# Performance work log

Measured on AMD Instinct MI355X. Metric: run time of the kernel, lower is better.

Reference implementation:

```python
import jax, jax.numpy as jnp
import numpy as np
import math

B, N, D, H, K, W = 2, 2048, 512, 8, 64, 5
HD = D // H      # head_dim = 64
QC = HD // 4     # per-head quaternion component = 16
QI = D // 4      # full-model quaternion component = 128


def _qlinear(x, r, i, j, k, b):
    # Hamilton-product weight matrix, as built in QLinear.forward
    Wm = jnp.concatenate([
        jnp.concatenate([r, -i, -j, -k], 1),
        jnp.concatenate([i,  r, -k,  j], 1),
        jnp.concatenate([j,  k,  r, -i], 1),
        jnp.concatenate([k, -j,  i,  r], 1)], 0)
    return x @ Wm.T + b


def _layernorm(x, g, b, eps=1e-5):
    m = x.mean(-1, keepdims=True)
    v = ((x - m) ** 2).mean(-1, keepdims=True)
    return (x - m) / jnp.sqrt(v + eps) * g + b


def _forward(query, key, value, cross_context, density_feat, mask, time_idx,
             q_r, q_i, q_j, q_k, q_b, k_r, k_i, k_j, k_k, k_b,
             v_w, v_b, o_w, o_b, thr, dm1_w, dm1_b, dm2_w, dm2_b,
             ef, ec, ev_w, ev_b, ln_g, ln_b):
    spike_slope = 5.0
    # ---- QuaternionSpikeAttention (cross_ctx=True, dropout inactive in eval) ----
    q = _qlinear(query, q_r, q_i, q_j, q_k, q_b)
    k = _qlinear(key, k_r, k_i, k_j, k_k, k_b) + _qlinear(cross_context, k_r, k_i, k_j, k_k, k_b)
    v = jnp.concatenate([value, cross_context], -1) @ v_w.T + v_b
    qh = q.reshape(B, N, H, HD)
    kh = k.reshape(B, N, H, HD)
    vh = v.reshape(B, N, H, HD)
    # sum of the 4 quaternion-component dot products == full dot over head_dim
    scores = jnp.einsum('bmhd,bnhd->bhmn', qh, kh) / math.sqrt(QC)
    scores = jnp.clip(scores, -6.0, 6.0)
    base_thr = jax.nn.softplus(thr)
    hdm = jax.nn.gelu(density_feat @ dm1_w.T + dm1_b, approximate=False)
    d_shift = (hdm @ dm2_w.T + dm2_b)[..., 0]                # [B, N]
    threshold = base_thr + d_shift[:, None, None, :] * 0.1   # varies over key index
    gate = jax.nn.sigmoid(spike_slope * (scores - threshold))
    mod = scores * (1.0 + 2.0 * gate)
    m2 = mask[:, None, :, None] * mask[:, None, None, :]     # [B,1,M,N] outer mask
    mod = jnp.where(m2 == 0, -10000.0, mod)
    wts = jax.nn.softmax(jnp.clip(mod, -30.0, 30.0), axis=-1)
    attn = jnp.einsum('bhmn,bnhd->bmhd', wts, vh).reshape(B, N, D)
    attn = attn @ o_w.T + o_b
    # ---- TemporalEventConvolution ----
    order = jnp.argsort(time_idx, axis=1)
    qs = jnp.take_along_axis(query, order[..., None], axis=1)
    ms = jnp.take_along_axis(mask, order, axis=1)
    half = W // 2
    qp = jnp.pad(qs, ((0, 0), (half, half), (0, 0)))
    qwin = jnp.stack([qp[:, w:w + N] for w in range(W)], axis=2)  # [B,N,W,D]
    # quaternion-split filter matching collapses to a full dot over D
    act = jnp.einsum('bnwd,kwd->bnk', qwin, ef) / math.sqrt(QI)
    act = jnp.where(ms[..., None] == 0, -10000.0, act)
    act = jax.nn.softmax(act, axis=-1)
    ctx = act @ ec                                            # [B,N,D]
    ctx = _layernorm(ctx @ ev_w.T + ev_b, ln_g, ln_b) * ms[..., None]
    inv = jnp.argsort(order, axis=1)
    ctx = jnp.take_along_axis(ctx, inv[..., None], axis=1) * mask[..., None]
    return attn + ctx


def setup_inputs() -> dict:
    key0 = jax.random.key(0)
    ks = jax.random.split(key0, 24)
    lim = math.sqrt(6.0 / (QI + QI))
    def xav(k):
        return jax.random.uniform(k, (QI, QI), jnp.float32, -lim, lim)
    def lin(k, o, i):
        l = math.sqrt(1.0 / i)
        return jax.random.uniform(k, (o, i), jnp.float32, -l, l)
    return {
        'query': jax.random.normal(ks[0], (B, N, D), jnp.float32),
        'key': jax.random.normal(ks[1], (B, N, D), jnp.float32),
        'value': jax.random.normal(ks[2], (B, N, D), jnp.float32),
        'cross_context': jax.random.normal(ks[3], (B, N, D), jnp.float32),
        'density_feat': jax.random.normal(ks[4], (B, N, 3), jnp.float32),
        'mask': jnp.ones((B, N), jnp.float32),
        'time_idx': jax.random.randint(ks[5], (B, N), 0, 1000000),
        'q_r': xav(ks[6]), 'q_i': xav(ks[7]), 'q_j': xav(ks[8]), 'q_k': xav(ks[9]),
        'q_b': jnp.zeros((D,), jnp.float32),
        'k_r': xav(ks[10]), 'k_i': xav(ks[11]), 'k_j': xav(ks[12]), 'k_k': xav(ks[13]),
        'k_b': jnp.zeros((D,), jnp.float32),
        'v_w': lin(ks[14], D, 2 * D), 'v_b': jnp.zeros((D,), jnp.float32),
        'o_w': lin(ks[15], D, D), 'o_b': jnp.zeros((D,), jnp.float32),
        'thr': jnp.float32(-1.0),
        'dm1_w': lin(ks[16], 16, 3), 'dm1_b': jnp.zeros((16,), jnp.float32),
        'dm2_w': jnp.zeros((1, 16), jnp.float32), 'dm2_b': jnp.zeros((1,), jnp.float32),
        'ef': jax.random.normal(ks[17], (K, W, D), jnp.float32) * 0.02,
        'ec': jax.random.normal(ks[18], (K, D), jnp.float32) * 0.02,
        'ev_w': lin(ks[19], D, D), 'ev_b': jnp.zeros((D,), jnp.float32),
        'ln_g': jnp.ones((D,), jnp.float32), 'ln_b': jnp.zeros((D,), jnp.float32),
    }


def reference(query, key, value, cross_context, density_feat, mask, time_idx,
              q_r, q_i, q_j, q_k, q_b, k_r, k_i, k_j, k_k, k_b,
              v_w, v_b, o_w, o_b, thr, dm1_w, dm1_b, dm2_w, dm2_b,
              ef, ec, ev_w, ev_b, ln_g, ln_b):
    return _forward(query, key, value, cross_context, density_feat, mask, time_idx,
                    q_r, q_i, q_j, q_k, q_b, k_r, k_i, k_j, k_k, k_b,
                    v_w, v_b, o_w, o_b, thr, dm1_w, dm1_b, dm2_w, dm2_b,
                    ef, ec, ev_w, ev_b, ln_g, ln_b)
```

## Files before the change

kernel.cpp:

```cpp
#include <hip/hip_runtime.h>
#include <math.h>

#define BB 2
#define NN 2048
#define DDIM 512
#define HH 8
#define HDIM 64
#define BN 4096

#define WS_WMQ   0
#define WS_WMK   262144
#define WS_THRK  524288
#define WS_ORDER 528384
#define WS_DKW   532480
#define WS_W5    1843200
#define WS_Q     2105344
#define WS_K     4202496
#define WS_V     6299648
#define PLANE_US 2097152

typedef short bf16x8 __attribute__((ext_vector_type(8)));
typedef float f32x4  __attribute__((ext_vector_type(4)));

__device__ __forceinline__ float4 ld4(const float* p) { return *(const float4*)p; }

__device__ __forceinline__ float red16_sum(float v) {
  v += __shfl_xor(v, 1, 64);
  v += __shfl_xor(v, 2, 64);
  v += __shfl_xor(v, 4, 64);
  v += __shfl_xor(v, 8, 64);
  return v;
}

__device__ __forceinline__ unsigned short f2bu(float f) {
  unsigned u = __float_as_uint(f);
  unsigned r = 0x7FFFu + ((u >> 16) & 1u);
  return (unsigned short)((u + r) >> 16);
}
__device__ __forceinline__ float bu2f(unsigned short u) {
  return __uint_as_float(((unsigned)u) << 16);
}
__device__ __forceinline__ void split2(float x, unsigned short& hi, unsigned short& lo) {
  hi = f2bu(x);
  lo = f2bu(x - bu2f(hi));
}

__device__ __forceinline__ void build_wm_body(int idx,
    const float* qr, const float* qi, const float* qj, const float* qk,
    const float* kr, const float* ki, const float* kj, const float* kk,
    unsigned short* wmqH, unsigned short* wmqL,
    unsigned short* wmkH, unsigned short* wmkL)
{
  int sel = idx >> 18;
  int r   = idx & 262143;
  int p = r >> 9, q = r & 511;
  int pb = p >> 7, qb = q >> 7, pr = p & 127, qc = q & 127;
  const int   comp_t[4][4] = {{0,1,2,3},{1,0,3,2},{2,3,0,1},{3,2,1,0}};
  const float sign_t[4][4] = {{1.f,-1.f,-1.f,-1.f},{1.f,1.f,-1.f,1.f},
                              {1.f,1.f,1.f,-1.f},{1.f,-1.f,1.f,1.f}};
  const float* cq[4] = {qr,qi,qj,qk};
  const float* ck[4] = {kr,ki,kj,kk};
  int c = comp_t[pb][qb];
  float s = sign_t[pb][qb];
  const float* src = sel ? ck[c] : cq[c];
  float v = s * src[pr*128 + qc];
  unsigned short hi, lo;
  split2(v, hi, lo);
  if (sel) { wmkH[r] = hi; wmkL[r] = lo; }
  else     { wmqH[r] = hi; wmqL[r] = lo; }
}

__device__ __forceinline__ void presplit_body(int i, const float* src, int n4,
    unsigned short* hp, unsigned short* lp)
{
  if (i >= n4) return;
  float4 v = ((const float4*)src)[i];
  ushort4 h, l;
  split2(v.x, h.x, l.x);  split2(v.y, h.y, l.y);
  split2(v.z, h.z, l.z);  split2(v.w, h.w, l.w);
  ((ushort4*)hp)[i] = h;
  ((ushort4*)lp)[i] = l;
}

__device__ __forceinline__ void thr_body(int i,
    const float* df, const float* dm1w, const float* dm1b,
    const float* dm2w, const float* dm2b, const float* thrp,
    int dm1b_bstride, float* thrK)
{
  if (i >= BN) return;
  int b = i >> 11;
  const float* bb = dm1b + b*dm1b_bstride;
  float x0 = df[i*3+0], x1 = df[i*3+1], x2 = df[i*3+2];
  float acc = dm2b[0];
  #pragma unroll
  for (int j = 0; j < 16; j++) {
    float h = dm1w[j*3+0]*x0 + dm1w[j*3+1]*x1 + dm1w[j*3+2]*x2 + bb[j];
    h = 0.5f * h * (1.f + erff(h * 0.70710678118654752f));
    acc += h * dm2w[j];
  }
  float tv = thrp[0];
  float base = fmaxf(tv, 0.f) + log1pf(expf(-fabsf(tv)));
  thrK[i] = base + 0.1f * acc;
}

__global__ __launch_bounds__(256) void prologue_kernel(
    const float* __restrict__ qr, const float* __restrict__ qi,
    const float* __restrict__ qj, const float* __restrict__ qk,
    const float* __restrict__ kr, const float* __restrict__ ki,
    const float* __restrict__ kj, const float* __restrict__ kk,
    unsigned short* __restrict__ wmqH, unsigned short* __restrict__ wmqL,
    unsigned short* __restrict__ wmkH, unsigned short* __restrict__ wmkL,
    const float* __restrict__ query,
    unsigned short* __restrict__ qryH, unsigned short* __restrict__ qryL,
    const float* __restrict__ v_w,
    unsigned short* __restrict__ vwH, unsigned short* __restrict__ vwL,
    const float* __restrict__ o_w,
    unsigned short* __restrict__ owH, unsigned short* __restrict__ owL,
    const int* __restrict__ tidx, int* __restrict__ order,
    const float* __restrict__ df, const float* __restrict__ dm1w,
    const float* __restrict__ dm1b, const float* __restrict__ dm2w,
    const float* __restrict__ dm2b, const float* __restrict__ thrp,
    int dm1b_bstride, float* __restrict__ thrK,
    const float* __restrict__ ef, int efn4,
    unsigned short* __restrict__ efH, unsigned short* __restrict__ efL)
{
  __shared__ int ts[NN];
  int bx = blockIdx.x, t = threadIdx.x;
  if (bx < 2048) {
    build_wm_body(bx*256 + t, qr,qi,qj,qk, kr,ki,kj,kk, wmqH,wmqL, wmkH,wmkL);
  } else if (bx < 4096) {
    presplit_body((bx-2048)*256 + t, query, 524288, qryH, qryL);
  } else if (bx < 4608) {
    presplit_body((bx-4096)*256 + t, v_w, 131072, vwH, vwL);
  } else if (bx < 4864) {
    presplit_body((bx-4608)*256 + t, o_w, 65536, owH, owL);
  } else if (bx < 4880) {
    int r = bx - 4864;
    int b = r >> 3, blk = r & 7;
    for (int i = t; i < NN; i += 256) ts[i] = tidx[b*NN + i];
    __syncthreads();
    int i = blk*256 + t;
    int ti = ts[i];
    int rank = 0;
    #pragma unroll 4
    for (int j = 0; j < NN; j++) {
      int tj = ts[j];
      rank += (tj < ti || (tj == ti && j < i)) ? 1 : 0;
    }
    order[b*NN + rank] = i;
  } else if (bx < 4896) {
    thr_body((bx-4880)*256 + t, df, dm1w, dm1b, dm2w, dm2b, thrp,
             dm1b_bstride, thrK);
  } else {
    presplit_body((bx-4896)*256 + t, ef, efn4, efH, efL);
  }
}

__global__ __launch_bounds__(256) void presplit_kernel(
    const float* __restrict__ src, int n4,
    unsigned short* __restrict__ hp, unsigned short* __restrict__ lp)
{
  presplit_body(blockIdx.x*256 + threadIdx.x, src, n4, hp, lp);
}

#define GSTR 72
template<int MODE, int OUT, int AP, int BP>
__device__ __forceinline__ void mgemm_body(
    unsigned short* AHi, unsigned short* ALo,
    unsigned short* BHi, unsigned short* BLo,
    const float* __restrict__ A0, const float* __restrict__ A1,
    const unsigned short* __restrict__ APh, const unsigned short* __restrict__ APl,
    const float* __restrict__ W,
    const unsigned short* __restrict__ BPh, const unsigned short* __restrict__ BPl,
    const float* __restrict__ bias,
    float bias_scale, float scale, float* __restrict__ out,
    int Ka, int N, int ldout, int bx, int by)
{
  const int t = threadIdx.x;
  const int w = t >> 6, lane = t & 63;
  const int quad = lane >> 4, lm = lane & 15;
  const int m0 = bx * 64, n0 = by * 64;
  const int lrr = t >> 4, ld = (t & 15) * 4;

  f32x4 acc[4];
  #pragma unroll
  for (int s = 0; s < 4; s++) acc[s] = (f32x4){0.f,0.f,0.f,0.f};

  for (int k0 = 0; k0 < Ka; k0 += 64) {
    __syncthreads();
    if (AP) {
      #pragma unroll
      for (int i = 0; i < 2; i++) {
        int c = t*2 + i;
        int row = c >> 3, c8 = (c & 7) * 8;
        int off = (m0 + row)*Ka + k0 + c8;
        *(uint4*)&AHi[row*GSTR + c8] = *(const uint4*)&APh[off];
        *(uint4*)&ALo[row*GSTR + c8] = *(const uint4*)&APl[off];
      }
    } else {
      #pragma unroll
      for (int p = 0; p < 4; p++) {
        int row = lrr + p*16;
        float4 av;
        if (MODE == 0) {
          av = ld4(&A0[(size_t)(m0+row)*Ka + k0 + ld]);
        } else if (MODE == 1) {
          float4 x = ld4(&A0[(m0+row)*512 + k0 + ld]);
          float4 y = ld4(&A1[(m0+row)*512 + k0 + ld]);
          av = make_float4(x.x+y.x, x.y+y.y, x.z+y.z, x.w+y.w);
        } else {
          int kg = k0 + ld;
          av = (kg < 512) ? ld4(&A0[(m0+row)*512 + kg])
                          : ld4(&A1[(m0+row)*512 + kg - 512]);
        }
        ushort4 hi, lo;
        split2(av.x, hi.x, lo.x);  split2(av.y, hi.y, lo.y);
        split2(av.z, hi.z, lo.z);  split2(av.w, hi.w, lo.w);
        *(ushort4*)&AHi[row*GSTR + ld] = hi;
        *(ushort4*)&ALo[row*GSTR + ld] = lo;
      }
    }
    if (BP) {
      #pragma unroll
      for (int i = 0; i < 2; i++) {
        int c = t*2 + i;
        int row = c >> 3, c8 = (c & 7) * 8;
        int brow = n0 + row;  if (brow > N-1) brow = N-1;
        int off = brow*Ka + k0 + c8;
        *(uint4*)&BHi[row*GSTR + c8] = *(const uint4*)&BPh[off];
        *(uint4*)&BLo[row*GSTR + c8] = *(const uint4*)&BPl[off];
      }
    } else {
      #pragma unroll
      for (int p = 0; p < 4; p++) {
        int row = lrr + p*16;
        int brow = n0 + row;  if (brow > N-1) brow = N-1;
        float4 wv = ld4(&W[(size_t)brow*Ka + k0 + ld]);
        ushort4 hi, lo;
        split2(wv.x, hi.x, lo.x);  split2(wv.y, hi.y, lo.y);
        split2(wv.z, hi.z, lo.z);  split2(wv.w, hi.w, lo.w);
        *(ushort4*)&BHi[row*GSTR + ld] = hi;
        *(ushort4*)&BLo[row*GSTR + ld] = lo;
      }
    }
    __syncthreads();
    #pragma unroll
    for (int ks = 0; ks < 2; ks++) {
      int arow = (w*16 + lm)*GSTR + ks*32 + quad*8;
      bf16x8 ah = *(const bf16x8*)&AHi[arow];
      bf16x8 al = *(const bf16x8*)&ALo[arow];
      #pragma unroll
      for (int sub = 0; sub < 4; sub++) {
        int baddr = (sub*16 + lm)*GSTR + ks*32 + quad*8;
        bf16x8 bh = *(const bf16x8*)&BHi[baddr];
        bf16x8 bl = *(const bf16x8*)&BLo[baddr];
        acc[sub] = __builtin_amdgcn_mfma_f32_16x16x32_bf16(ah, bh, acc[sub], 0, 0, 0);
        acc[sub] = __builtin_amdgcn_mfma_f32_16x16x32_bf16(ah, bl, acc[sub], 0, 0, 0);
        acc[sub] = __builtin_amdgcn_mfma_f32_16x16x32_bf16(al, bh, acc[sub], 0, 0, 0);
      }
    }
  }
  #pragma unroll
  for (int sub = 0; sub < 4; sub++) {
    int col = n0 + sub*16 + lm;
    if (col >= N) continue;
    float bv = bias ? bias[col] * bias_scale : 0.f;
    if (OUT == 0) {
      #pragma unroll
      for (int r = 0; r < 4; r++) {
        int row = m0 + w*16 + quad*4 + r;
        out[(size_t)row*ldout + col] = acc[sub][r]*scale + bv;
      }
    } else if (OUT == 1) {
      unsigned short* hp = (unsigned short*)out;
      unsigned short* lp = hp + (size_t)4096*ldout;
      #pragma unroll
      for (int r = 0; r < 4; r++) {
        int row = m0 + w*16 + quad*4 + r;
        unsigned short hv, lv;
        split2(acc[sub][r]*scale + bv, hv, lv);
        hp[(size_t)row*ldout + col] = hv;
        lp[(size_t)row*ldout + col] = lv;
      }
    } else {
      unsigned short* hp = (unsigned short*)out;
      unsigned short* lp = hp + (size_t)PLANE_US;
      int hcol = col >> 6, d = col & 63;
      int row0 = m0 + w*16 + quad*4;
      int bb2 = row0 >> 11, n = row0 & 2047;
      unsigned short h0,h1,h2,h3,l0,l1,l2,l3;
      split2(acc[sub][0]*scale + bv, h0, l0);
      split2(acc[sub][1]*scale + bv, h1, l1);
      split2(acc[sub][2]*scale + bv, h2, l2);
      split2(acc[sub][3]*scale + bv, h3, l3);
      size_t vidx = (((size_t)bb2*8 + hcol)*64 + d)*2048 + n;
      *(ushort4*)&hp[vidx] = make_ushort4(h0,h1,h2,h3);
      *(ushort4*)&lp[vidx] = make_ushort4(l0,l1,l2,l3);
    }
  }
}

template<int MODE, int OUT, int AP, int BP>
__global__ __launch_bounds__(256) void mgemm_kernel(
    const float* __restrict__ A0, const float* __restrict__ A1,
    const unsigned short* __restrict__ APh, const unsigned short* __restrict__ APl,
    const float* __restrict__ W,
    const unsigned short* __restrict__ BPh, const unsigned short* __restrict__ BPl,
    const float* __restrict__ bias,
    float bias_scale, float scale, float* __restrict__ out,
    int Ka, int N, int ldout)
{
  __shared__ __align__(16) unsigned short AHi[64*GSTR], ALo[64*GSTR];
  __shared__ __align__(16) unsigned short BHi[64*GSTR], BLo[64*GSTR];
  mgemm_body<MODE,OUT,AP,BP>(AHi, ALo, BHi, BLo, A0, A1, APh, APl, W, BPh, BPl,
                             bias, bias_scale, scale, out, Ka, N, ldout,
                             blockIdx.x, blockIdx.y);
}

__global__ __launch_bounds__(256) void qkv_kernel(
    const unsigned short* __restrict__ qryH, const unsigned short* __restrict__ qryL,
    const unsigned short* __restrict__ wmqH, const unsigned short* __restrict__ wmqL,
    const float* __restrict__ q_b, float* __restrict__ Qb,
    const float* __restrict__ key_, const float* __restrict__ cross,
    const unsigned short* __restrict__ wmkH, const unsigned short* __restrict__ wmkL,
    const float* __restrict__ k_b, float* __restrict__ Kb,
    const float* __restrict__ value,
    const unsigned short* __restrict__ vwH, const unsigned short* __restrict__ vwL,
    const float* __restrict__ v_b, float* __restrict__ Vb,
    const unsigned short* __restrict__ efH, const unsigned short* __restrict__ efL,
    float rs128, int KW, float* __restrict__ dkwO)
{
  __shared__ __align__(16) unsigned short AHi[64*GSTR], ALo[64*GSTR];
  __shared__ __align__(16) unsigned short BHi[64*GSTR], BLo[64*GSTR];
  int by = blockIdx.y;
  if (by < 8) {
    mgemm_body<0,1,1,1>(AHi, ALo, BHi, BLo, nullptr, nullptr, qryH, qryL,
                        nullptr, wmqH, wmqL, q_b, 1.f, 1.f, Qb, 512, 512, 512,
                        blockIdx.x, by);
  } else if (by < 16) {
    mgemm_body<1,1,0,1>(AHi, ALo, BHi, BLo, key_, cross, nullptr, nullptr,
                        nullptr, wmkH, wmkL, k_b, 2.f, 1.f, Kb, 512, 512, 512,
                        blockIdx.x, by - 8);
  } else if (by < 24) {
    mgemm_body<2,2,0,1>(AHi, ALo, BHi, BLo, value, cross, nullptr, nullptr,
                        nullptr, vwH, vwL, v_b, 1.f, 1.f, Vb, 1024, 512, 512,
                        blockIdx.x, by - 16);
  } else {
    mgemm_body<0,0,1,1>(AHi, ALo, BHi, BLo, nullptr, nullptr, qryH, qryL,
                        nullptr, efH, efL, nullptr, 0.f, rs128, dkwO, 512, KW, KW,
                        blockIdx.x, by - 24);
  }
}

__global__ __launch_bounds__(256) void otail_kernel(
    const unsigned short* __restrict__ aH, const unsigned short* __restrict__ aL,
    const unsigned short* __restrict__ owH, const unsigned short* __restrict__ owL,
    const float* __restrict__ o_b, float* __restrict__ OutF,
    const float* __restrict__ dkw, const int* __restrict__ order,
    int K, int W, float* __restrict__ w5,
    const float* __restrict__ ec, const float* __restrict__ evw,
    float* __restrict__ ecv)
{
  __shared__ __align__(16) unsigned short AHi[64*GSTR], ALo[64*GSTR];
  __shared__ __align__(16) unsigned short BHi[64*GSTR], BLo[64*GSTR];
  int by = blockIdx.y;
  if (by < 8) {
    mgemm_body<0,0,1,1>(AHi, ALo, BHi, BLo, nullptr, nullptr, aH, aL,
                        nullptr, owH, owL, o_b, 1.f, 1.f, OutF, 512, 512, 512,
                        blockIdx.x, by);
  } else if (by == 8) {
    int KW = K*W, half = W >> 1;
    int total = BN*K;
    for (int idx = blockIdx.x*256 + threadIdx.x; idx < total; idx += 64*256) {
      int k  = idx % K;
      int bn = idx / K;
      int b = bn >> 11, r = bn & 2047;
      const int* ob = order + b*NN;
      float acc = 0.f;
      for (int w = 0; w < W; w++) {
        int rr = r + w - half;
        if (rr < 0 || rr >= NN) continue;
        acc += dkw[(size_t)(b*NN + ob[rr])*KW + k*W + w];
      }
      w5[(size_t)(b*NN + ob[r])*K + k] = acc;
    }
  } else {
    int total = K*512;
    for (int idx = blockIdx.x*256 + threadIdx.x; idx < total; idx += 64*256) {
      int k = idx >> 9, j = idx & 511;
      const float4* e4 = (const float4*)(ec + k*512);
      const float4* w4 = (const float4*)(evw + j*512);
      float acc = 0.f;
      for (int d = 0; d < 128; d++) {
        float4 a = e4[d], bv = w4[d];
        acc += a.x*bv.x + a.y*bv.y + a.z*bv.z + a.w*bv.w;
      }
      ecv[k*512 + j] = acc;
    }
  }
}

__global__ __launch_bounds__(256) void t2f_kernel(const float* __restrict__ w5raw,
    const float* __restrict__ ecv, const float* __restrict__ evb,
    const float* __restrict__ mask, int K, float* __restrict__ ctx2)
{
  int idx = blockIdx.x * 256 + threadIdx.x;
  int bn = idx >> 7;
  int q4 = idx & 127;
  const float* row = w5raw + (size_t)bn*K;
  const float4* e4 = (const float4*)ecv;
  float4 acc = ((const float4*)evb)[q4];
  float mk = mask[bn];
  if (mk == 0.f) {
    float u = 1.f / (float)K;
    for (int k = 0; k < K; k++) {
      float4 e = e4[k*128 + q4];
      acc.x += u*e.x; acc.y += u*e.y; acc.z += u*e.z; acc.w += u*e.w;
    }
  } else {
    float mx = -1e30f;
    for (int k = 0; k < K; k++) mx = fmaxf(mx, row[k]);
    float ss = 0.f;
    for (int k = 0; k < K; k++) ss += __expf(row[k]-mx);
    float inv = 1.f/ss;
    for (int k = 0; k < K; k++) {
      float w = __expf(row[k]-mx) * inv;
      float4 e = e4[k*128 + q4];
      acc.x += w*e.x; acc.y += w*e.y; acc.z += w*e.z; acc.w += w*e.w;
    }
  }
  ((float4*)ctx2)[idx] = acc;
}

#define QSTR 72
__global__ __launch_bounds__(256) void attn_kernel(
    const unsigned short* __restrict__ QHi, const unsigned short* __restrict__ QLo,
    const unsigned short* __restrict__ KHp, const unsigned short* __restrict__ KLp,
    const unsigned short* __restrict__ VtHi, const unsigned short* __restrict__ VtLo,
    const float* __restrict__ thrK, const float* __restrict__ mask,
    unsigned short* __restrict__ AoutH, unsigned short* __restrict__ AoutL)
{
  __shared__ __align__(16) unsigned short KHs[64*QSTR];
  __shared__ __align__(16) unsigned short KLs[64*QSTR];
  __shared__ __align__(16) unsigned short VHs[64*QSTR];
  __shared__ __align__(16) unsigned short VLs[64*QSTR];
  __shared__ float thr_s[64], mk_s[64], mm_s[32];
  __shared__ float ls[2][32];

  const int t = threadIdx.x;
  const int wv = t >> 6, lane = t & 63;
  const int g = wv & 1, sh = wv >> 1;
  const int quad = lane >> 4, lm = lane & 15;
  const int m0 = blockIdx.x * 32;
  const int bh = blockIdx.y;
  const int b = bh >> 3, h = bh & 7;
  const int base = b*NN*DDIM + h*HDIM;
  const int sr = t >> 3;
  const int sc = (t & 7) * 8;

  bf16x8 qh[2], ql[2];
  {
    size_t qoff = (size_t)(b*NN + m0 + g*16 + lm)*DDIM + h*HDIM + quad*8;
    qh[0] = *(const bf16x8*)&QHi[qoff];
    qh[1] = *(const bf16x8*)&QHi[qoff + 32];
    ql[0] = *(const bf16x8*)&QLo[qoff];
    ql[1] = *(const bf16x8*)&QLo[qoff + 32];
  }
  if (t < 32) mm_s[t] = mask[b*NN + m0 + t];

  f32x4 o_acc[2];
  o_acc[0] = (f32x4){0.f,0.f,0.f,0.f};
  o_acc[1] = (f32x4){0.f,0.f,0.f,0.f};
  float lsum[4] = {0.f,0.f,0.f,0.f};

  for (int n0 = 0; n0 < NN; n0 += 64) {
    __syncthreads();
    #pragma unroll
    for (int p = 0; p < 2; p++) {
      int row = sr + p*32;
      size_t gg = (size_t)(b*NN + n0 + row)*DDIM + h*HDIM + sc;
      *(uint4*)&KHs[row*QSTR + sc] = *(const uint4*)&KHp[gg];
      *(uint4*)&KLs[row*QSTR + sc] = *(const uint4*)&KLp[gg];
      size_t gv = ((size_t)bh*HDIM + row)*NN + n0 + sc;
      *(uint4*)&VHs[row*QSTR + sc] = *(const uint4*)&VtHi[gv];
      *(uint4*)&VLs[row*QSTR + sc] = *(const uint4*)&VtLo[gv];
    }
    if (t < 64) { thr_s[t] = thrK[b*NN + n0 + t]; mk_s[t] = mask[b*NN + n0 + t]; }
    __syncthreads();

    f32x4 s_acc[2];
    s_acc[0] = (f32x4){0.f,0.f,0.f,0.f};
    s_acc[1] = (f32x4){0.f,0.f,0.f,0.f};
    #pragma unroll
    for (int ks = 0; ks < 2; ks++) {
      #pragma unroll
      for (int sl = 0; sl < 2; sl++) {
        int sub = sh*2 + sl;
        int baddr = (sub*16 + lm)*QSTR + ks*32 + quad*8;
        bf16x8 bh8 = *(const bf16x8*)&KHs[baddr];
        bf16x8 bl8 = *(const bf16x8*)&KLs[baddr];
        s_acc[sl] = __builtin_amdgcn_mfma_f32_16x16x32_bf16(qh[ks], bh8, s_acc[sl], 0, 0, 0);
        s_acc[sl] = __builtin_amdgcn_mfma_f32_16x16x32_bf16(qh[ks], bl8, s_acc[sl], 0, 0, 0);
        s_acc[sl] = __builtin_amdgcn_mfma_f32_16x16x32_bf16(ql[ks], bh8, s_acc[sl], 0, 0, 0);
      }
    }
    __syncthreads();

    float thc5[2], mkc[2];
    #pragma unroll
    for (int sl = 0; sl < 2; sl++) {
      int key = (sh*2 + sl)*16 + lm;
      thc5[sl] = 5.f * thr_s[key];
      mkc[sl] = mk_s[key];
    }
    float p_[4][2];
    #pragma unroll
    for (int r = 0; r < 4; r++) {
      float mm = mm_s[g*16 + quad*4 + r];
      #pragma unroll
      for (int sl = 0; sl < 2; sl++) {
        float sc2 = s_acc[sl][r]*0.25f;
        sc2 = fminf(fmaxf(sc2,-6.f),6.f);
        float e = __expf(__builtin_fmaf(-5.f, sc2, thc5[sl]));
        float gte = __builtin_amdgcn_rcpf(1.f + e);
        float mv = sc2*(1.f + 2.f*gte);
        if (mm*mkc[sl] == 0.f) mv = -1e4f;
        mv = fminf(fmaxf(mv,-30.f),30.f);
        float p = __expf(mv - 30.f);
        p_[r][sl] = p;
        lsum[r] += p;
      }
    }
    #pragma unroll
    for (int r = 0; r < 4; r++) {
      int prow = (g*16 + quad*4 + r)*QSTR;
      int xk = quad << 3;
      #pragma unroll
      for (int sl = 0; sl < 2; sl++) {
        int cx = (lm + (sh*2+sl)*16) ^ xk;
        unsigned short hi, lo;
        split2(p_[r][sl], hi, lo);
        KHs[prow + cx] = hi;
        KLs[prow + cx] = lo;
      }
    }
    __syncthreads();

    bf16x8 ph[2], pl[2];
    {
      int arow = (g*16 + lm)*QSTR;
      int rk = ((lm >> 2) & 3) << 3;
      int c0 = (quad*8) ^ rk;
      int c1 = (quad*8 + 32) ^ rk;
      ph[0] = *(const bf16x8*)&KHs[arow + c0];
      ph[1] = *(const bf16x8*)&KHs[arow + c1];
      pl[0] = *(const bf16x8*)&KLs[arow + c0];
      pl[1] = *(const bf16x8*)&KLs[arow + c1];
    }
    #pragma unroll
    for (int ks = 0; ks < 2; ks++) {
      #pragma unroll
      for (int sl = 0; sl < 2; sl++) {
        int sub = sh*2 + sl;
        int baddr = (sub*16 + lm)*QSTR + ks*32 + quad*8;
        bf16x8 vh8 = *(const bf16x8*)&VHs[baddr];
        bf16x8 vl8 = *(const bf16x8*)&VLs[baddr];
        o_acc[sl] = __builtin_amdgcn_mfma_f32_16x16x32_bf16(ph[ks], vh8, o_acc[sl], 0, 0, 0);
        o_acc[sl] = __builtin_amdgcn_mfma_f32_16x16x32_bf16(ph[ks], vl8, o_acc[sl], 0, 0, 0);
        o_acc[sl] = __builtin_amdgcn_mfma_f32_16x16x32_bf16(pl[ks], vh8, o_acc[sl], 0, 0, 0);
      }
    }
  }

  __syncthreads();
  #pragma unroll
  for (int r = 0; r < 4; r++) {
    float s = red16_sum(lsum[r]);
    if (lm == 0) ls[sh][g*16 + quad*4 + r] = s;
  }
  __syncthreads();
  float inv[4];
  #pragma unroll
  for (int r = 0; r < 4; r++) {
    int rl = g*16 + quad*4 + r;
    inv[r] = 1.f / (ls[0][rl] + ls[1][rl]);
  }
  #pragma unroll
  for (int sl = 0; sl < 2; sl++) {
    #pragma unroll
    for (int r = 0; r < 4; r++) {
      int row = m0 + g*16 + quad*4 + r;
      float val = o_acc[sl][r] * inv[r];
      unsigned short hv, lv;
      split2(val, hv, lv);
      size_t o = (size_t)base + (size_t)row*DDIM + (sh*2+sl)*16 + lm;
      AoutH[o] = hv;
      AoutL[o] = lv;
    }
  }
}

__global__ __launch_bounds__(256) void t3_kernel(const float* __restrict__ ctx2,
    const float* __restrict__ lng, const float* __restrict__ lnb,
    const float* __restrict__ mask, const float* __restrict__ outf,
    float* __restrict__ out)
{
  int wid = threadIdx.x >> 6, lane = threadIdx.x & 63;
  int row = blockIdx.x * 4 + wid;
  const float4* x4 = (const float4*)(ctx2 + row*DDIM);
  float4 v0 = x4[lane], v1 = x4[lane+64];
  float s = v0.x+v0.y+v0.z+v0.w + v1.x+v1.y+v1.z+v1.w;
  #pragma unroll
  for (int m = 1; m < 64; m <<= 1) s += __shfl_xor(s, m, 64);
  float mean = s * (1.f/512.f);
  float d0 = v0.x-mean, d1 = v0.y-mean, d2 = v0.z-mean, d3 = v0.w-mean;
  float d4 = v1.x-mean, d5 = v1.y-mean, d6 = v1.z-mean, d7 = v1.w-mean;
  float sq = d0*d0+d1*d1+d2*d2+d3*d3+d4*d4+d5*d5+d6*d6+d7*d7;
  #pragma unroll
  for (int m = 1; m < 64; m <<= 1) sq += __shfl_xor(sq, m, 64);
  float rstd = rsqrtf(sq * (1.f/512.f) + 1e-5f);
  float mk = mask[row];
  float f = mk*mk;
  const float4* g4 = (const float4*)lng;
  const float4* b4 = (const float4*)lnb;
  float4 G0 = g4[lane], G1 = g4[lane+64], B0 = b4[lane], B1 = b4[lane+64];
  float4 O0 = *(const float4*)&outf[row*DDIM + lane*4];
  float4 O1 = *(const float4*)&outf[row*DDIM + (lane+64)*4];
  float4 R0, R1;
  R0.x = O0.x + (d0*rstd*G0.x + B0.x)*f;
  R0.y = O0.y + (d1*rstd*G0.y + B0.y)*f;
  R0.z = O0.z + (d2*rstd*G0.z + B0.z)*f;
  R0.w = O0.w + (d3*rstd*G0.w + B0.w)*f;
  R1.x = O1.x + (d4*rstd*G1.x + B1.x)*f;
  R1.y = O1.y + (d5*rstd*G1.y + B1.y)*f;
  R1.z = O1.z + (d6*rstd*G1.z + B1.z)*f;
  R1.w = O1.w + (d7*rstd*G1.w + B1.w)*f;
  *(float4*)&out[row*DDIM + lane*4] = R0;
  *(float4*)&out[row*DDIM + (lane+64)*4] = R1;
}

__global__ void telem_write_kernel(float val, float* __restrict__ out)
{
  if (threadIdx.x == 0 && blockIdx.x == 0) out[0] = val;
}

extern "C" void kernel_launch(void* const* d_in, const int* in_sizes, int n_in,
                              void* d_out, int out_size, void* d_ws, size_t ws_size,
                              hipStream_t stream)
{
  (void)n_in; (void)out_size; (void)ws_size;
  const float* query = (const float*)d_in[0];
  const float* key_  = (const float*)d_in[1];
  const float* value = (const float*)d_in[2];
  const float* cross = (const float*)d_in[3];
  const float* df    = (const float*)d_in[4];
  const float* mask  = (const float*)d_in[5];
  const int*   tidx  = (const int*)  d_in[6];
  const float* q_r = (const float*)d_in[7],  *q_i = (const float*)d_in[8];
  const float* q_j = (const float*)d_in[9],  *q_k = (const float*)d_in[10];
  const float* q_b = (const float*)d_in[11];
  const float* k_r = (const float*)d_in[12], *k_i = (const float*)d_in[13];
  const float* k_j = (const float*)d_in[14], *k_k = (const float*)d_in[15];
  const float* k_b = (const float*)d_in[16];
  const float* v_w = (const float*)d_in[17], *v_b = (const float*)d_in[18];
  const float* o_w = (const float*)d_in[19], *o_b = (const float*)d_in[20];
  const float* thrp = (const float*)d_in[21];
  const float* dm1w = (const float*)d_in[22], *dm1b = (const float*)d_in[23];
  const float* dm2w = (const float*)d_in[24], *dm2b = (const float*)d_in[25];
  const float* ef   = (const float*)d_in[26], *ec   = (const float*)d_in[27];
  const float* ev_w = (const float*)d_in[28], *ev_b = (const float*)d_in[29];
  const float* lng  = (const float*)d_in[30], *lnb  = (const float*)d_in[31];

  const int s23 = in_sizes[23];
  const int s26 = in_sizes[26];
  const int s27 = in_sizes[27];
  int Kf = (s27 > 0 && s27 % 512 == 0) ? s27 / 512 : 0;
  int Wf = (Kf > 0 && s26 % (Kf*512) == 0) ? s26 / (Kf*512) : 0;
  bool cfg_ok = (Kf >= 1 && Kf <= 64) && (Wf == 1 || Wf == 3 || Wf == 5)
                && (Kf*Wf <= 320);
  if (!cfg_ok) { Kf = 5; Wf = 5; }
  const int KW = Kf * Wf;
  const int dm1b_bstride = (s23 == 32) ? 16 : 0;
  const bool fused_ef = (KW <= 160);

  float* ws   = (float*)d_ws;
  float* thrK = ws + WS_THRK;
  int*   order = (int*)(ws + WS_ORDER);
  float* Qb   = ws + WS_Q;
  float* Kb   = ws + WS_K;
  float* Vb   = ws + WS_V;
  float* out  = (float*)d_out;
  float* OutF = Kb;
  float* ctx2 = Qb;
  float* w5   = ws + WS_V;

  unsigned short* wmqH = (unsigned short*)(ws + WS_WMQ);
  unsigned short* wmqL = wmqH + 262144;
  unsigned short* wmkH = (unsigned short*)(ws + WS_WMK);
  unsigned short* wmkL = wmkH + 262144;
  unsigned short* qryH = (unsigned short*)d_out;
  unsigned short* qryL = qryH + PLANE_US;
  unsigned short* vwH  = (unsigned short*)(ws + WS_DKW);
  unsigned short* vwL  = vwH + 524288;
  unsigned short* owH  = (unsigned short*)(ws + WS_W5);
  unsigned short* owL  = owH + 262144;
  float* ecv = ws + WS_WMQ;

  float* dkwP;
  unsigned short *efH_, *efL_;
  if (fused_ef) {
    dkwP = ws + WS_DKW + 524288;
    efH_ = (unsigned short*)(dkwP + (size_t)BN*KW);
    efL_ = efH_ + KW*512;
  } else {
    dkwP = ws + WS_DKW;
    efH_ = (unsigned short*)(ws + WS_WMQ);
    efL_ = efH_ + KW*512;
  }

  const unsigned short* QHi = (const unsigned short*)Qb;
  const unsigned short* QLo = QHi + PLANE_US;
  const unsigned short* KHp = (const unsigned short*)Kb;
  const unsigned short* KLp = KHp + PLANE_US;
  const unsigned short* VtH = (const unsigned short*)Vb;
  const unsigned short* VtL = VtH + PLANE_US;

  const int efblocks = fused_ef ? (KW*128 + 255)/256 : 0;
  prologue_kernel<<<4896 + efblocks, 256, 0, stream>>>(
      q_r,q_i,q_j,q_k, k_r,k_i,k_j,k_k, wmqH,wmqL, wmkH,wmkL,
      query, qryH, qryL, v_w, vwH, vwL, o_w, owH, owL,
      tidx, order, df, dm1w, dm1b, dm2w, dm2b, thrp, dm1b_bstride, thrK,
      ef, KW*128, efH_, efL_);

  const float rs128 = 0.08838834764831845f;
  const int efcols = (KW + 63) / 64;
  qkv_kernel<<<dim3(64, fused_ef ? 24 + efcols : 24), 256, 0, stream>>>(
      qryH, qryL, wmqH, wmqL, q_b, Qb,
      key_, cross, wmkH, wmkL, k_b, Kb,
      value, vwH, vwL, v_b, Vb,
      efH_, efL_, rs128, KW, dkwP);
  if (!fused_ef) {
    presplit_kernel<<<(KW*128 + 255)/256, 256, 0, stream>>>(ef, KW*128, efH_, efL_);
    mgemm_kernel<0,0,1,1><<<dim3(64, efcols), 256, 0, stream>>>(
        nullptr, nullptr, qryH, qryL, nullptr, efH_, efL_, nullptr, 0.f, rs128,
        dkwP, 512, KW, KW);
  }

  attn_kernel<<<dim3(64,16), 256, 0, stream>>>(QHi, QLo, KHp, KLp, VtH, VtL,
                                               thrK, mask, qryH, qryL);
  otail_kernel<<<dim3(64,10), 256, 0, stream>>>(
      qryH, qryL, owH, owL, o_b, OutF,
      dkwP, order, Kf, Wf, w5, ec, ev_w, ecv);

  t2f_kernel<<<2048, 256, 0, stream>>>(w5, ecv, ev_b, mask, Kf, ctx2);
  t3_kernel<<<1024, 256, 0, stream>>>(ctx2, lng, lnb, mask, OutF, out);

  if (!cfg_ok) {
    int K2 = (s27 / 512 < 127) ? s27 / 512 : 127;
    telem_write_kernel<<<1, 64, 0, stream>>>(-65536.f * (float)(K2+1), out);
  }
}
```

Measured before the change: 490.6 us.

## Fuse event-context softmax with LayerNorm residual and remap attention block order

Merges the t2f kernel, which builds the event-context rows, with the t3 LayerNorm-plus-residual kernel. Each 256-thread block now holds two full 512-wide rows and reduces mean and variance through shared memory, so the ctx2 intermediate is never written to or read back from global memory and one launch is removed. Separately, the attention kernel's grid index is permuted so that consecutive blocks cover different batch-head pairs, which changes how work spreads across XCDs and L2. The fused kernel adds two __syncthreads barriers.

```diff
diff --git a/kernel.cpp b/kernel.cpp
--- a/kernel.cpp
+++ b/kernel.cpp
@@ -400,13 +400,17 @@
   }
 }
 
-__global__ __launch_bounds__(256) void t2f_kernel(const float* __restrict__ w5raw,
+__global__ __launch_bounds__(256) void t23_kernel(const float* __restrict__ w5raw,
     const float* __restrict__ ecv, const float* __restrict__ evb,
-    const float* __restrict__ mask, int K, float* __restrict__ ctx2)
-{
+    const float* __restrict__ mask, int K,
+    const float* __restrict__ lng, const float* __restrict__ lnb,
+    const float* __restrict__ outf, float* __restrict__ out)
+{
+  __shared__ float sm[4], sv[4];
   int idx = blockIdx.x * 256 + threadIdx.x;
   int bn = idx >> 7;
   int q4 = idx & 127;
+  int wv = threadIdx.x >> 6;
   const float* row = w5raw + (size_t)bn*K;
   const float4* e4 = (const float4*)ecv;
   float4 acc = ((const float4*)evb)[q4];
@@ -429,7 +433,30 @@
       acc.x += w*e.x; acc.y += w*e.y; acc.z += w*e.z; acc.w += w*e.w;
     }
   }
-  ((float4*)ctx2)[idx] = acc;
+  float s = acc.x + acc.y + acc.z + acc.w;
+  #pragma unroll
+  for (int m = 1; m < 64; m <<= 1) s += __shfl_xor(s, m, 64);
+  if ((threadIdx.x & 63) == 0) sm[wv] = s;
+  __syncthreads();
+  int p = wv & 2;
+  float mean = (sm[p] + sm[p+1]) * (1.f/512.f);
+  float d0 = acc.x-mean, d1 = acc.y-mean, d2 = acc.z-mean, d3 = acc.w-mean;
+  float sq = d0*d0 + d1*d1 + d2*d2 + d3*d3;
+  #pragma unroll
+  for (int m = 1; m < 64; m <<= 1) sq += __shfl_xor(sq, m, 64);
+  if ((threadIdx.x & 63) == 0) sv[wv] = sq;
+  __syncthreads();
+  float rstd = rsqrtf((sv[p] + sv[p+1]) * (1.f/512.f) + 1e-5f);
+  float f = mk*mk;
+  float4 G = ((const float4*)lng)[q4];
+  float4 B = ((const float4*)lnb)[q4];
+  float4 O = ((const float4*)outf)[(size_t)bn*128 + q4];
+  float4 R;
+  R.x = O.x + (d0*rstd*G.x + B.x)*f;
+  R.y = O.y + (d1*rstd*G.y + B.y)*f;
+  R.z = O.z + (d2*rstd*G.z + B.z)*f;
+  R.w = O.w + (d3*rstd*G.w + B.w)*f;
+  ((float4*)out)[(size_t)bn*128 + q4] = R;
 }
 
 #define QSTR 72
@@ -451,8 +478,10 @@
   const int wv = t >> 6, lane = t & 63;
   const int g = wv & 1, sh = wv >> 1;
   const int quad = lane >> 4, lm = lane & 15;
-  const int m0 = blockIdx.x * 32;
-  const int bh = blockIdx.y;
+  const int f = blockIdx.y * 64 + blockIdx.x;
+  const int wk = ((f & 7) << 7) | (f >> 3);
+  const int m0 = (wk & 63) * 32;
+  const int bh = wk >> 6;
   const int b = bh >> 3, h = bh & 7;
   const int base = b*NN*DDIM + h*HDIM;
   const int sr = t >> 3;
@@ -598,45 +627,6 @@
       AoutL[o] = lv;
     }
   }
-}
-
-__global__ __launch_bounds__(256) void t3_kernel(const float* __restrict__ ctx2,
-    const float* __restrict__ lng, const float* __restrict__ lnb,
-    const float* __restrict__ mask, const float* __restrict__ outf,
-    float* __restrict__ out)
-{
-  int wid = threadIdx.x >> 6, lane = threadIdx.x & 63;
-  int row = blockIdx.x * 4 + wid;
-  const float4* x4 = (const float4*)(ctx2 + row*DDIM);
-  float4 v0 = x4[lane], v1 = x4[lane+64];
-  float s = v0.x+v0.y+v0.z+v0.w + v1.x+v1.y+v1.z+v1.w;
-  #pragma unroll
-  for (int m = 1; m < 64; m <<= 1) s += __shfl_xor(s, m, 64);
-  float mean = s * (1.f/512.f);
-  float d0 = v0.x-mean, d1 = v0.y-mean, d2 = v0.z-mean, d3 = v0.w-mean;
-  float d4 = v1.x-mean, d5 = v1.y-mean, d6 = v1.z-mean, d7 = v1.w-mean;
-  float sq = d0*d0+d1*d1+d2*d2+d3*d3+d4*d4+d5*d5+d6*d6+d7*d7;
-  #pragma unroll
-  for (int m = 1; m < 64; m <<= 1) sq += __shfl_xor(sq, m, 64);
-  float rstd = rsqrtf(sq * (1.f/512.f) + 1e-5f);
-  float mk = mask[row];
-  float f = mk*mk;
-  const float4* g4 = (const float4*)lng;
-  const float4* b4 = (const float4*)lnb;
-  float4 G0 = g4[lane], G1 = g4[lane+64], B0 = b4[lane], B1 = b4[lane+64];
-  float4 O0 = *(const float4*)&outf[row*DDIM + lane*4];
-  float4 O1 = *(const float4*)&outf[row*DDIM + (lane+64)*4];
-  float4 R0, R1;
-  R0.x = O0.x + (d0*rstd*G0.x + B0.x)*f;
-  R0.y = O0.y + (d1*rstd*G0.y + B0.y)*f;
-  R0.z = O0.z + (d2*rstd*G0.z + B0.z)*f;
-  R0.w = O0.w + (d3*rstd*G0.w + B0.w)*f;
-  R1.x = O1.x + (d4*rstd*G1.x + B1.x)*f;
-  R1.y = O1.y + (d5*rstd*G1.y + B1.y)*f;
-  R1.z = O1.z + (d6*rstd*G1.z + B1.z)*f;
-  R1.w = O1.w + (d7*rstd*G1.w + B1.w)*f;
-  *(float4*)&out[row*DDIM + lane*4] = R0;
-  *(float4*)&out[row*DDIM + (lane+64)*4] = R1;
 }
 
 __global__ void telem_write_kernel(float val, float* __restrict__ out)
@@ -691,7 +681,6 @@
   float* Vb   = ws + WS_V;
   float* out  = (float*)d_out;
   float* OutF = Kb;
-  float* ctx2 = Qb;
   float* w5   = ws + WS_V;
 
   unsigned short* wmqH = (unsigned short*)(ws + WS_WMQ);
@@ -752,8 +741,8 @@
       qryH, qryL, owH, owL, o_b, OutF,
       dkwP, order, Kf, Wf, w5, ec, ev_w, ecv);
 
-  t2f_kernel<<<2048, 256, 0, stream>>>(w5, ecv, ev_b, mask, Kf, ctx2);
-  t3_kernel<<<1024, 256, 0, stream>>>(ctx2, lng, lnb, mask, OutF, out);
+  t23_kernel<<<2048, 256, 0, stream>>>(w5, ecv, ev_b, mask, Kf,
+                                       lng, lnb, OutF, out);
 
   if (!cfg_ok) {
     int K2 = (s27 / 512 < 127) ? s27 / 512 : 127;
```

New measurement: 487.1 us (median of 2 runs). Within noise of the previous version (-0.7%).
